# Kernel tuning notes

Hardware: AMD Instinct MI355X
Metric: run time of the kernel (lower is better)

## Reference

```python
import jax, jax.numpy as jnp
import numpy as np

B, V, C, CD, D, H, W = 1, 3, 32, 8, 32, 128, 160
LAMB = 1.5


def _bilinear(img, x, y):
    # img: [c, Hs, Ws]; x, y: pixel coords [D, HW]; zero padding, align_corners=True semantics
    c, Hs, Ws = img.shape
    x0 = jnp.floor(x)
    y0 = jnp.floor(y)
    x0i = x0.astype(jnp.int32)
    y0i = y0.astype(jnp.int32)
    wx = x - x0
    wy = y - y0
    imgf = img.reshape(c, Hs * Ws)

    def gather(xi, yi, w):
        valid = (xi >= 0) & (xi < Ws) & (yi >= 0) & (yi < Hs)
        lin = jnp.clip(yi, 0, Hs - 1) * Ws + jnp.clip(xi, 0, Ws - 1)
        v = jnp.take(imgf, lin.reshape(-1), axis=1).reshape((c,) + xi.shape)
        return v * (w * valid.astype(w.dtype))[None]

    return (gather(x0i, y0i, (1 - wx) * (1 - wy))
            + gather(x0i + 1, y0i, wx * (1 - wy))
            + gather(x0i, y0i + 1, (1 - wx) * wy)
            + gather(x0i + 1, y0i + 1, wx * wy))


def _homo_warp(src_fea, src_proj, ref_proj, depth_values):
    # src_fea [B,c,Hs,Ws]; projs [B,4,4]; depth_values [B,D,H,W] -> [B,c,D,H,W]
    b, c, Hs, Ws = src_fea.shape
    _, d, h, w = depth_values.shape
    proj = jnp.einsum('bij,bjk->bik', src_proj, jnp.linalg.inv(ref_proj))
    rot = proj[:, :3, :3]
    tr = proj[:, :3, 3]
    ys, xs = jnp.meshgrid(jnp.arange(h, dtype=src_fea.dtype), jnp.arange(w, dtype=src_fea.dtype), indexing='ij')
    xyz = jnp.stack([xs.reshape(-1), ys.reshape(-1), jnp.ones(h * w, dtype=src_fea.dtype)], 0)  # [3,HW]
    rx = jnp.einsum('bij,jn->bin', rot, xyz)  # [B,3,HW]
    dvals = depth_values.reshape(b, 1, d, h * w)
    pxyz = rx[:, :, None, :] * dvals + tr[:, :, None, None]  # [B,3,D,HW]
    z = pxyz[:, 2]
    px = pxyz[:, 0] / z  # [B,D,HW]
    py = pxyz[:, 1] / z
    out = jax.vmap(_bilinear)(src_fea, px, py)  # [B,c,D,HW]
    return out.reshape(b, c, d, h, w)


def setup_inputs() -> dict:
    key = jax.random.key(0)
    k1, k2, k3 = jax.random.split(key, 3)
    features = jax.random.normal(k1, (V, B, C, H, W), jnp.float32)
    deps_feature_stage = jax.random.normal(k2, (V, B, CD, H, W), jnp.float32)
    reg_w = jax.random.normal(k3, (1, C + CD), jnp.float32) * 0.1
    K = np.array([[200., 0., W / 2.], [0., 200., H / 2.], [0., 0., 1.]])
    mats = []
    for tx in [0.0, 1.0, -1.0]:
        Rt = np.eye(4)
        Rt[0, 3] = tx
        P = np.eye(4)
        P[:3, :4] = K @ Rt[:3, :4]
        mats.append(P)
    proj_matrices = jnp.asarray(np.stack(mats)[None], jnp.float32)  # [B,V,4,4]
    depth_values = jnp.broadcast_to(
        jnp.linspace(5.0, 10.0, D, dtype=jnp.float32)[None, :, None, None], (B, D, H, W)) + jnp.zeros((B, D, H, W), jnp.float32)
    return {'features': features, 'deps_feature_stage': deps_feature_stage,
            'proj_matrices': proj_matrices, 'depth_values': depth_values,
            'reg_w': reg_w, 'num_depth': D, 'stage_idx': 0}


def reference(features, deps_feature_stage, proj_matrices, depth_values, reg_w, num_depth, stage_idx):
    num_views = features.shape[0]
    d = depth_values.shape[1]
    ref_proj = proj_matrices[:, 0]

    def variance_volume(feats):
        ref = feats[0]  # [B,c,H,W]
        ref_vol = jnp.broadcast_to(ref[:, :, None], (ref.shape[0], ref.shape[1], d, ref.shape[2], ref.shape[3]))
        s = ref_vol
        sq = ref_vol * ref_vol
        for v in range(1, num_views):
            wv = _homo_warp(feats[v], proj_matrices[:, v], ref_proj, depth_values)
            s = s + wv
            sq = sq + wv * wv
        return sq / num_views - (s / num_views) ** 2

    volume_variance = variance_volume(features)      # [B,C,D,H,W]
    deps_variance = variance_volume(deps_feature_stage)  # [B,CD,D,H,W]
    var = jnp.concatenate([volume_variance, deps_variance], axis=1)
    # cost_regularization modeled as 1x1x1 conv reducing channels to 1
    cost = jnp.einsum('bcdhw,oc->bodhw', var, reg_w)[:, 0]  # [B,D,H,W]
    prob_volume = jax.nn.softmax(cost, axis=1)
    depth = jnp.sum(prob_volume * depth_values, axis=1)  # [B,H,W]
    samp_variance = (depth_values - depth[:, None]) ** 2
    exp_variance = LAMB * jnp.sqrt(jnp.sum(samp_variance * prob_volume, axis=1))
    return depth, exp_variance, prob_volume
```

## Files before the change

### kernel.cpp

```cpp
#include <hip/hip_runtime.h>
#include <hip/hip_fp16.h>
#include <math.h>

#define HH   128
#define WW   160
#define HWN  (HH*WW)
#define NCF  32
#define NCD  8
#define ND   32
#define NV   3
#define LAMBF 1.5f

template <int CH>
__device__ void transpose_tile(const float* __restrict__ src, __half* __restrict__ dst,
                               float (*lds)[33], int tid) {
    for (int i = tid; i < CH*8; i += 256) {
        int c = i >> 3, xg = (i & 7) << 2;
        *(float4*)&lds[c][xg] = *(const float4*)(src + c*HWN + xg);
    }
    __syncthreads();
    for (int i = tid; i < 32*(CH/4); i += 256) {
        int xl = i / (CH/4), c4 = (i % (CH/4)) * 4;
        __half2 h0 = __floats2half2_rn(lds[c4][xl],   lds[c4+1][xl]);
        __half2 h1 = __floats2half2_rn(lds[c4+2][xl], lds[c4+3][xl]);
        uint2 u; u.x = *(unsigned*)&h0; u.y = *(unsigned*)&h1;
        *(uint2*)(dst + xl*CH + c4) = u;
    }
}

__global__ __launch_bounds__(256) void prep_k(const float* __restrict__ feat,
                                              const float* __restrict__ deps,
                                              const float* __restrict__ proj,
                                              __half* __restrict__ featH,
                                              __half* __restrict__ depsH,
                                              float* __restrict__ projw) {
    if (blockIdx.x == 0 && blockIdx.y == 0 && blockIdx.z == 0 && threadIdx.x == 0) {
        float M00 = proj[0], M01 = proj[1], M02 = proj[2],  m0 = proj[3];
        float M10 = proj[4], M11 = proj[5], M12 = proj[6],  m1 = proj[7];
        float M20 = proj[8], M21 = proj[9], M22 = proj[10], m2 = proj[11];
        float c00 =  (M11*M22 - M12*M21);
        float c01 = -(M10*M22 - M12*M20);
        float c02 =  (M10*M21 - M11*M20);
        float det = M00*c00 + M01*c01 + M02*c02;
        float id  = 1.f / det;
        float i00 = c00*id, i01 = -(M01*M22 - M02*M21)*id, i02 =  (M01*M12 - M02*M11)*id;
        float i10 = c01*id, i11 =  (M00*M22 - M02*M20)*id, i12 = -(M00*M12 - M02*M10)*id;
        float i20 = c02*id, i21 = -(M00*M21 - M01*M20)*id, i22 =  (M00*M11 - M01*M10)*id;
        float t0 = -(i00*m0 + i01*m1 + i02*m2);
        float t1 = -(i10*m0 + i11*m1 + i12*m2);
        float t2 = -(i20*m0 + i21*m1 + i22*m2);
        #pragma unroll
        for (int v = 1; v < NV; v++) {
            const float* S = proj + v*16;
            float s00 = S[0], s01 = S[1], s02 = S[2],  st0 = S[3];
            float s10 = S[4], s11 = S[5], s12 = S[6],  st1 = S[7];
            float s20 = S[8], s21 = S[9], s22 = S[10], st2 = S[11];
            float* o = projw + (v-1)*12;
            o[0] = s00*i00 + s01*i10 + s02*i20;
            o[1] = s00*i01 + s01*i11 + s02*i21;
            o[2] = s00*i02 + s01*i12 + s02*i22;
            o[3] = s10*i00 + s11*i10 + s12*i20;
            o[4] = s10*i01 + s11*i11 + s12*i21;
            o[5] = s10*i02 + s11*i12 + s12*i22;
            o[6] = s20*i00 + s21*i10 + s22*i20;
            o[7] = s20*i01 + s21*i11 + s22*i21;
            o[8] = s20*i02 + s21*i12 + s22*i22;
            o[9]  = s00*t0 + s01*t1 + s02*t2 + st0;
            o[10] = s10*t0 + s11*t1 + s12*t2 + st1;
            o[11] = s20*t0 + s21*t1 + s22*t2 + st2;
        }
    }

    __shared__ float lds[NCF][33];
    const int z  = blockIdx.z;
    const int xb = blockIdx.x * 32;
    const int y  = blockIdx.y;
    if (z < NV) {
        transpose_tile<NCF>(feat + (size_t)(z*NCF)*HWN + y*WW + xb,
                            featH + (size_t)(z*HWN + y*WW + xb) * NCF,
                            lds, threadIdx.x);
    } else {
        transpose_tile<NCD>(deps + (size_t)((z - NV)*NCD)*HWN + y*WW + xb,
                            depsH + (size_t)((z - NV)*HWN + y*WW + xb) * NCD,
                            lds, threadIdx.x);
    }
}

__global__ __launch_bounds__(256) void cost_volume_k(
    const __half* __restrict__ featH,
    const __half* __restrict__ depsH,
    const float* __restrict__ dvals,
    const float* __restrict__ regw,
    const float* __restrict__ pws,
    float* __restrict__ out)
{
    __shared__ float cl [ND][9];
    __shared__ float dvl[ND][9];
    __shared__ float smax[8], sisum[8];

    const int t    = threadIdx.x;
    const int lane = t & 63;
    const int wid  = t >> 6;
    const int cg   = lane & 7;
    const int pl   = lane >> 3;
    const int pixg = blockIdx.x * 8 + pl;
    const int y    = pixg / WW;
    const int x    = pixg - y * WW;
    const float fx = (float)x, fy = (float)y;
    const int dbase = wid * 8;
    const int plbase = lane & 0x38;

    float RX[2], RY[2], RZ[2], T0[2], T1[2], T2[2];
    #pragma unroll
    for (int v = 0; v < 2; v++) {
        const float* q = pws + v*12;
        RX[v] = q[0]*fx + q[1]*fy + q[2];
        RY[v] = q[3]*fx + q[4]*fy + q[5];
        RZ[v] = q[6]*fx + q[7]*fy + q[8];
        T0[v] = q[9]; T1[v] = q[10]; T2[v] = q[11];
    }

    int SW00[2], SW10[2], SW01[2], SW11[2];
    int SO00[2], SO10[2], SO01[2], SO11[2];
    {
        float dvv_own = dvals[(dbase + cg)*HWN + pixg];
        dvl[dbase + cg][pl] = dvv_own;
        #pragma unroll
        for (int v = 0; v < 2; v++) {
            float pz = RZ[v]*dvv_own + T2[v];
            float iz = __builtin_amdgcn_rcpf(pz);
            float px = (RX[v]*dvv_own + T0[v]) * iz;
            float py = (RY[v]*dvv_own + T1[v]) * iz;
            float x0f = floorf(px), y0f = floorf(py);
            int x0 = (int)x0f, y0 = (int)y0f;
            float wx = px - x0f, wy = py - y0f;
            float omx = 1.f - wx, omy = 1.f - wy;
            bool vx0 = (x0 >= 0) & (x0 < WW);
            bool vx1 = (x0+1 >= 0) & (x0+1 < WW);
            bool vy0 = (y0 >= 0) & (y0 < HH);
            bool vy1 = (y0+1 >= 0) & (y0+1 < HH);
            float W00 = (vx0 && vy0) ? omx*omy : 0.f;
            float W10 = (vx1 && vy0) ? wx*omy  : 0.f;
            float W01 = (vx0 && vy1) ? omx*wy  : 0.f;
            float W11 = (vx1 && vy1) ? wx*wy   : 0.f;
            __half2 h;
            h = __float2half2_rn(W00); SW00[v] = *(int*)&h;
            h = __float2half2_rn(W10); SW10[v] = *(int*)&h;
            h = __float2half2_rn(W01); SW01[v] = *(int*)&h;
            h = __float2half2_rn(W11); SW11[v] = *(int*)&h;
            int xc0 = min(max(x0,   0), WW-1);
            int xc1 = min(max(x0+1, 0), WW-1);
            int yc0 = min(max(y0,   0), HH-1);
            int yc1 = min(max(y0+1, 0), HH-1);
            SO00[v] = (yc0*WW + xc0)*NCF;
            SO10[v] = (yc0*WW + xc1)*NCF;
            SO01[v] = (yc1*WW + xc0)*NCF;
            SO11[v] = (yc1*WW + xc1)*NCF;
        }
    }

    #define INTERP(BPTR, O00, O10, O01, O11, W00p, W10p, W01p, W11p)          \
        {                                                                      \
            uint2 u00 = *(const uint2*)(BPTR + O00);                           \
            uint2 u10 = *(const uint2*)(BPTR + O10);                           \
            uint2 u01 = *(const uint2*)(BPTR + O01);                           \
            uint2 u11 = *(const uint2*)(BPTR + O11);                           \
            __half2 wva = __hmul2(*(__half2*)&u00.x, W00p);                    \
            wva = __hfma2(*(__half2*)&u10.x, W10p, wva);                       \
            wva = __hfma2(*(__half2*)&u01.x, W01p, wva);                       \
            wva = __hfma2(*(__half2*)&u11.x, W11p, wva);                       \
            __half2 wvb = __hmul2(*(__half2*)&u00.y, W00p);                    \
            wvb = __hfma2(*(__half2*)&u10.y, W10p, wvb);                       \
            wvb = __hfma2(*(__half2*)&u01.y, W01p, wvb);                       \
            wvb = __hfma2(*(__half2*)&u11.y, W11p, wvb);                       \
            float2 fa = __half22float2(wva);                                   \
            float2 fb = __half22float2(wvb);                                   \
            s0 += fa.x; q0 = fmaf(fa.x, fa.x, q0);                             \
            s1 += fa.y; q1 = fmaf(fa.y, fa.y, q1);                             \
            s2 += fb.x; q2 = fmaf(fb.x, fb.x, q2);                             \
            s3 += fb.y; q3 = fmaf(fb.y, fb.y, q3);                             \
        }

    {
        uint2 ur = *(const uint2*)(featH + (size_t)pixg*NCF + cg*4);
        float2 ra = __half22float2(*(__half2*)&ur.x);
        float2 rb = __half22float2(*(__half2*)&ur.y);
        const float rx0 = ra.x, rx1 = ra.y, rx2 = rb.x, rx3 = rb.y;
        const float4 w4 = *(const float4*)(regw + cg*4);
        const float wca0 = w4.x*(1.f/3.f), wca1 = w4.y*(1.f/3.f),
                    wca2 = w4.z*(1.f/3.f), wca3 = w4.w*(1.f/3.f);
        const float wcb0 = w4.x*(1.f/9.f), wcb1 = w4.y*(1.f/9.f),
                    wcb2 = w4.z*(1.f/9.f), wcb3 = w4.w*(1.f/9.f);
        const __half* b1 = featH + (size_t)1*HWN*NCF + cg*4;
        const __half* b2 = featH + (size_t)2*HWN*NCF + cg*4;

        #pragma unroll 2
        for (int jj = 0; jj < 8; jj++) {
            const int src = plbase | jj;
            float s0 = rx0, s1 = rx1, s2 = rx2, s3 = rx3;
            float q0 = rx0*rx0, q1 = rx1*rx1, q2 = rx2*rx2, q3 = rx3*rx3;

            #pragma unroll
            for (int v = 0; v < 2; v++) {
                int w00i = __shfl(SW00[v], src, 64);
                int w10i = __shfl(SW10[v], src, 64);
                int w01i = __shfl(SW01[v], src, 64);
                int w11i = __shfl(SW11[v], src, 64);
                int o00  = __shfl(SO00[v], src, 64);
                int o10  = __shfl(SO10[v], src, 64);
                int o01  = __shfl(SO01[v], src, 64);
                int o11  = __shfl(SO11[v], src, 64);
                __half2 W00p = *(__half2*)&w00i, W10p = *(__half2*)&w10i;
                __half2 W01p = *(__half2*)&w01i, W11p = *(__half2*)&w11i;
                const __half* b = v ? b2 : b1;
                INTERP(b, o00, o10, o01, o11, W00p, W10p, W01p, W11p)
            }
            float part = wca0*q0 - wcb0*s0*s0;
            part = fmaf(wca1, q1, part); part = fmaf(-wcb1, s1*s1, part);
            part = fmaf(wca2, q2, part); part = fmaf(-wcb2, s2*s2, part);
            part = fmaf(wca3, q3, part); part = fmaf(-wcb3, s3*s3, part);
            part += __shfl_xor(part, 1);
            part += __shfl_xor(part, 2);
            part += __shfl_xor(part, 4);
            if (cg == jj) cl[dbase + jj][pl] = part;
        }
    }

    {
        const int cgd  = lane & 1;
        const int dsub = (lane >> 1) & 3;
        uint2 ur = *(const uint2*)(depsH + (size_t)pixg*NCD + cgd*4);
        float2 ra = __half22float2(*(__half2*)&ur.x);
        float2 rb = __half22float2(*(__half2*)&ur.y);
        const float rx0 = ra.x, rx1 = ra.y, rx2 = rb.x, rx3 = rb.y;
        const float4 w4 = *(const float4*)(regw + NCF + cgd*4);
        const float wca0 = w4.x*(1.f/3.f), wca1 = w4.y*(1.f/3.f),
                    wca2 = w4.z*(1.f/3.f), wca3 = w4.w*(1.f/3.f);
        const float wcb0 = w4.x*(1.f/9.f), wcb1 = w4.y*(1.f/9.f),
                    wcb2 = w4.z*(1.f/9.f), wcb3 = w4.w*(1.f/9.f);
        const __half* b1 = depsH + (size_t)1*HWN*NCD + cgd*4;
        const __half* b2 = depsH + (size_t)2*HWN*NCD + cgd*4;

        #pragma unroll
        for (int i = 0; i < 2; i++) {
            const int jj = dsub + 4*i;
            const int d  = dbase + jj;
            const int src = plbase | jj;
            float s0 = rx0, s1 = rx1, s2 = rx2, s3 = rx3;
            float q0 = rx0*rx0, q1 = rx1*rx1, q2 = rx2*rx2, q3 = rx3*rx3;

            #pragma unroll
            for (int v = 0; v < 2; v++) {
                int w00i = __shfl(SW00[v], src, 64);
                int w10i = __shfl(SW10[v], src, 64);
                int w01i = __shfl(SW01[v], src, 64);
                int w11i = __shfl(SW11[v], src, 64);
                int o00  = __shfl(SO00[v], src, 64) >> 2;
                int o10  = __shfl(SO10[v], src, 64) >> 2;
                int o01  = __shfl(SO01[v], src, 64) >> 2;
                int o11  = __shfl(SO11[v], src, 64) >> 2;
                __half2 W00p = *(__half2*)&w00i, W10p = *(__half2*)&w10i;
                __half2 W01p = *(__half2*)&w01i, W11p = *(__half2*)&w11i;
                const __half* b = v ? b2 : b1;
                INTERP(b, o00, o10, o01, o11, W00p, W10p, W01p, W11p)
            }
            float part = wca0*q0 - wcb0*s0*s0;
            part = fmaf(wca1, q1, part); part = fmaf(-wcb1, s1*s1, part);
            part = fmaf(wca2, q2, part); part = fmaf(-wcb2, s2*s2, part);
            part = fmaf(wca3, q3, part); part = fmaf(-wcb3, s3*s3, part);
            part += __shfl_xor(part, 1);
            if (cgd == 0) cl[d][pl] += part;
        }
    }
    __syncthreads();

    if (t < 8) {
        const int plx  = t;
        const int pixo = blockIdx.x * 8 + plx;
        float m = -1e30f;
        #pragma unroll
        for (int d = 0; d < ND; d++) m = fmaxf(m, cl[d][plx]);
        float sum = 0.f, pd = 0.f, pd2 = 0.f;
        #pragma unroll
        for (int d = 0; d < ND; d++) {
            float e   = __expf(cl[d][plx] - m);
            float dvv = dvl[d][plx];
            sum += e;
            pd  = fmaf(e, dvv, pd);
            pd2 = fmaf(e, dvv*dvv, pd2);
        }
        float isum  = 1.f / sum;
        float depth = pd * isum;
        float sv    = pd2 * isum - depth*depth;
        float ev    = LAMBF * sqrtf(fmaxf(sv, 0.f));
        smax[plx]  = m;
        sisum[plx] = isum;
        out[pixo]       = depth;
        out[HWN + pixo] = ev;
    }
    __syncthreads();
    {
        const int plx  = t & 7;
        const int dd   = t >> 3;
        const int pixo = blockIdx.x * 8 + plx;
        out[2*HWN + dd*HWN + pixo] = __expf(cl[dd][plx] - smax[plx]) * sisum[plx];
    }
}

extern "C" void kernel_launch(void* const* d_in, const int* in_sizes, int n_in,
                              void* d_out, int out_size, void* d_ws, size_t ws_size,
                              hipStream_t stream) {
    const float* features = (const float*)d_in[0];
    const float* deps     = (const float*)d_in[1];
    const float* proj     = (const float*)d_in[2];
    const float* dvals    = (const float*)d_in[3];
    const float* regw     = (const float*)d_in[4];

    float*  ws    = (float*)d_ws;
    float*  projw = ws;
    __half* featH = (__half*)(ws + 64);
    __half* depsH = featH + (size_t)NV*HWN*NCF;

    dim3 tg(WW/32, HH, 2*NV);
    prep_k<<<tg, 256, 0, stream>>>(features, deps, proj, featH, depsH, projw);

    cost_volume_k<<<HWN/8, 256, 0, stream>>>(featH, depsH, dvals, regw, projw,
                                             (float*)d_out);
}
```

Before: 103.0 us.

## Widen per-lane channel loads to 16 bytes and give the deps stage one depth per lane

The main feature stage now has each lane handle 8 half channels with uint4 loads and process two depths per group of 8 lanes, which halves the loop count and drops one shuffle-reduction step. The deps stage is restructured so each lane owns a whole depth and all 8 deps channels, using its own precomputed offsets and weights without any shuffles or cross-lane reduction. The goal is fewer, wider gather instructions and less shuffle overhead. The cost is more registers per thread, which may reduce occupancy.

```diff
diff --git a/kernel.cpp b/kernel.cpp
--- a/kernel.cpp
+++ b/kernel.cpp
@@ -101,7 +101,8 @@
     const int t    = threadIdx.x;
     const int lane = t & 63;
     const int wid  = t >> 6;
-    const int cg   = lane & 7;
+    const int cg2  = lane & 3;
+    const int dp   = (lane >> 2) & 1;
     const int pl   = lane >> 3;
     const int pixg = blockIdx.x * 8 + pl;
     const int y    = pixg / WW;
@@ -123,8 +124,8 @@
     int SW00[2], SW10[2], SW01[2], SW11[2];
     int SO00[2], SO10[2], SO01[2], SO11[2];
     {
-        float dvv_own = dvals[(dbase + cg)*HWN + pixg];
-        dvl[dbase + cg][pl] = dvv_own;
+        float dvv_own = dvals[(dbase + (lane & 7))*HWN + pixg];
+        dvl[dbase + (lane & 7)][pl] = dvv_own;
         #pragma unroll
         for (int v = 0; v < 2; v++) {
             float pz = RZ[v]*dvv_own + T2[v];
@@ -159,46 +160,48 @@
         }
     }
 
-    #define INTERP(BPTR, O00, O10, O01, O11, W00p, W10p, W01p, W11p)          \
-        {                                                                      \
-            uint2 u00 = *(const uint2*)(BPTR + O00);                           \
-            uint2 u10 = *(const uint2*)(BPTR + O10);                           \
-            uint2 u01 = *(const uint2*)(BPTR + O01);                           \
-            uint2 u11 = *(const uint2*)(BPTR + O11);                           \
-            __half2 wva = __hmul2(*(__half2*)&u00.x, W00p);                    \
-            wva = __hfma2(*(__half2*)&u10.x, W10p, wva);                       \
-            wva = __hfma2(*(__half2*)&u01.x, W01p, wva);                       \
-            wva = __hfma2(*(__half2*)&u11.x, W11p, wva);                       \
-            __half2 wvb = __hmul2(*(__half2*)&u00.y, W00p);                    \
-            wvb = __hfma2(*(__half2*)&u10.y, W10p, wvb);                       \
-            wvb = __hfma2(*(__half2*)&u01.y, W01p, wvb);                       \
-            wvb = __hfma2(*(__half2*)&u11.y, W11p, wvb);                       \
-            float2 fa = __half22float2(wva);                                   \
-            float2 fb = __half22float2(wvb);                                   \
-            s0 += fa.x; q0 = fmaf(fa.x, fa.x, q0);                             \
-            s1 += fa.y; q1 = fmaf(fa.y, fa.y, q1);                             \
-            s2 += fb.x; q2 = fmaf(fb.x, fb.x, q2);                             \
-            s3 += fb.y; q3 = fmaf(fb.y, fb.y, q3);                             \
-        }
+    #define H2OF(u, k) (((const __half2*)&(u))[k])
+    #define INTERP8(u00, u10, u01, u11, W00p, W10p, W01p, W11p)                \
+        { _Pragma("unroll")                                                    \
+          for (int k = 0; k < 4; k++) {                                        \
+            __half2 wv = __hmul2(H2OF(u00,k), W00p);                           \
+            wv = __hfma2(H2OF(u10,k), W10p, wv);                               \
+            wv = __hfma2(H2OF(u01,k), W01p, wv);                               \
+            wv = __hfma2(H2OF(u11,k), W11p, wv);                               \
+            float2 f = __half22float2(wv);                                     \
+            s[2*k]   += f.x; q[2*k]   = fmaf(f.x, f.x, q[2*k]);                \
+            s[2*k+1] += f.y; q[2*k+1] = fmaf(f.y, f.y, q[2*k+1]);              \
+          } }
 
     {
-        uint2 ur = *(const uint2*)(featH + (size_t)pixg*NCF + cg*4);
-        float2 ra = __half22float2(*(__half2*)&ur.x);
-        float2 rb = __half22float2(*(__half2*)&ur.y);
-        const float rx0 = ra.x, rx1 = ra.y, rx2 = rb.x, rx3 = rb.y;
-        const float4 w4 = *(const float4*)(regw + cg*4);
-        const float wca0 = w4.x*(1.f/3.f), wca1 = w4.y*(1.f/3.f),
-                    wca2 = w4.z*(1.f/3.f), wca3 = w4.w*(1.f/3.f);
-        const float wcb0 = w4.x*(1.f/9.f), wcb1 = w4.y*(1.f/9.f),
-                    wcb2 = w4.z*(1.f/9.f), wcb3 = w4.w*(1.f/9.f);
-        const __half* b1 = featH + (size_t)1*HWN*NCF + cg*4;
-        const __half* b2 = featH + (size_t)2*HWN*NCF + cg*4;
+        uint4 ur = *(const uint4*)(featH + (size_t)pixg*NCF + cg2*8);
+        float rx[8];
+        {
+            float2 f;
+            f = __half22float2(H2OF(ur,0)); rx[0]=f.x; rx[1]=f.y;
+            f = __half22float2(H2OF(ur,1)); rx[2]=f.x; rx[3]=f.y;
+            f = __half22float2(H2OF(ur,2)); rx[4]=f.x; rx[5]=f.y;
+            f = __half22float2(H2OF(ur,3)); rx[6]=f.x; rx[7]=f.y;
+        }
+        float wca[8], wcb[8];
+        {
+            float4 wa = *(const float4*)(regw + cg2*8);
+            float4 wb = *(const float4*)(regw + cg2*8 + 4);
+            wca[0]=wa.x*(1.f/3.f); wca[1]=wa.y*(1.f/3.f); wca[2]=wa.z*(1.f/3.f); wca[3]=wa.w*(1.f/3.f);
+            wca[4]=wb.x*(1.f/3.f); wca[5]=wb.y*(1.f/3.f); wca[6]=wb.z*(1.f/3.f); wca[7]=wb.w*(1.f/3.f);
+            wcb[0]=wa.x*(1.f/9.f); wcb[1]=wa.y*(1.f/9.f); wcb[2]=wa.z*(1.f/9.f); wcb[3]=wa.w*(1.f/9.f);
+            wcb[4]=wb.x*(1.f/9.f); wcb[5]=wb.y*(1.f/9.f); wcb[6]=wb.z*(1.f/9.f); wcb[7]=wb.w*(1.f/9.f);
+        }
+        const __half* b1 = featH + (size_t)1*HWN*NCF + cg2*8;
+        const __half* b2 = featH + (size_t)2*HWN*NCF + cg2*8;
 
         #pragma unroll 2
-        for (int jj = 0; jj < 8; jj++) {
+        for (int jp = 0; jp < 4; jp++) {
+            const int jj  = (dp << 2) | jp;
             const int src = plbase | jj;
-            float s0 = rx0, s1 = rx1, s2 = rx2, s3 = rx3;
-            float q0 = rx0*rx0, q1 = rx1*rx1, q2 = rx2*rx2, q3 = rx3*rx3;
+            float s[8], q[8];
+            #pragma unroll
+            for (int i = 0; i < 8; i++) { s[i] = rx[i]; q[i] = rx[i]*rx[i]; }
 
             #pragma unroll
             for (int v = 0; v < 2; v++) {
@@ -213,64 +216,70 @@
                 __half2 W00p = *(__half2*)&w00i, W10p = *(__half2*)&w10i;
                 __half2 W01p = *(__half2*)&w01i, W11p = *(__half2*)&w11i;
                 const __half* b = v ? b2 : b1;
-                INTERP(b, o00, o10, o01, o11, W00p, W10p, W01p, W11p)
+                uint4 u00 = *(const uint4*)(b + o00);
+                uint4 u10 = *(const uint4*)(b + o10);
+                uint4 u01 = *(const uint4*)(b + o01);
+                uint4 u11 = *(const uint4*)(b + o11);
+                INTERP8(u00, u10, u01, u11, W00p, W10p, W01p, W11p)
             }
-            float part = wca0*q0 - wcb0*s0*s0;
-            part = fmaf(wca1, q1, part); part = fmaf(-wcb1, s1*s1, part);
-            part = fmaf(wca2, q2, part); part = fmaf(-wcb2, s2*s2, part);
-            part = fmaf(wca3, q3, part); part = fmaf(-wcb3, s3*s3, part);
+            float part = wca[0]*q[0] - wcb[0]*s[0]*s[0];
+            #pragma unroll
+            for (int i = 1; i < 8; i++) {
+                part = fmaf(wca[i], q[i], part);
+                part = fmaf(-wcb[i], s[i]*s[i], part);
+            }
             part += __shfl_xor(part, 1);
             part += __shfl_xor(part, 2);
-            part += __shfl_xor(part, 4);
-            if (cg == jj) cl[dbase + jj][pl] = part;
+            if (cg2 == 0) cl[dbase + jj][pl] = part;
         }
     }
 
     {
-        const int cgd  = lane & 1;
-        const int dsub = (lane >> 1) & 3;
-        uint2 ur = *(const uint2*)(depsH + (size_t)pixg*NCD + cgd*4);
-        float2 ra = __half22float2(*(__half2*)&ur.x);
-        float2 rb = __half22float2(*(__half2*)&ur.y);
-        const float rx0 = ra.x, rx1 = ra.y, rx2 = rb.x, rx3 = rb.y;
-        const float4 w4 = *(const float4*)(regw + NCF + cgd*4);
-        const float wca0 = w4.x*(1.f/3.f), wca1 = w4.y*(1.f/3.f),
-                    wca2 = w4.z*(1.f/3.f), wca3 = w4.w*(1.f/3.f);
-        const float wcb0 = w4.x*(1.f/9.f), wcb1 = w4.y*(1.f/9.f),
-                    wcb2 = w4.z*(1.f/9.f), wcb3 = w4.w*(1.f/9.f);
-        const __half* b1 = depsH + (size_t)1*HWN*NCD + cgd*4;
-        const __half* b2 = depsH + (size_t)2*HWN*NCD + cgd*4;
-
-        #pragma unroll
-        for (int i = 0; i < 2; i++) {
-            const int jj = dsub + 4*i;
-            const int d  = dbase + jj;
-            const int src = plbase | jj;
-            float s0 = rx0, s1 = rx1, s2 = rx2, s3 = rx3;
-            float q0 = rx0*rx0, q1 = rx1*rx1, q2 = rx2*rx2, q3 = rx3*rx3;
-
-            #pragma unroll
-            for (int v = 0; v < 2; v++) {
-                int w00i = __shfl(SW00[v], src, 64);
-                int w10i = __shfl(SW10[v], src, 64);
-                int w01i = __shfl(SW01[v], src, 64);
-                int w11i = __shfl(SW11[v], src, 64);
-                int o00  = __shfl(SO00[v], src, 64) >> 2;
-                int o10  = __shfl(SO10[v], src, 64) >> 2;
-                int o01  = __shfl(SO01[v], src, 64) >> 2;
-                int o11  = __shfl(SO11[v], src, 64) >> 2;
-                __half2 W00p = *(__half2*)&w00i, W10p = *(__half2*)&w10i;
-                __half2 W01p = *(__half2*)&w01i, W11p = *(__half2*)&w11i;
-                const __half* b = v ? b2 : b1;
-                INTERP(b, o00, o10, o01, o11, W00p, W10p, W01p, W11p)
-            }
-            float part = wca0*q0 - wcb0*s0*s0;
-            part = fmaf(wca1, q1, part); part = fmaf(-wcb1, s1*s1, part);
-            part = fmaf(wca2, q2, part); part = fmaf(-wcb2, s2*s2, part);
-            part = fmaf(wca3, q3, part); part = fmaf(-wcb3, s3*s3, part);
-            part += __shfl_xor(part, 1);
-            if (cgd == 0) cl[d][pl] += part;
-        }
+        const int d = dbase + (lane & 7);
+        uint4 ur = *(const uint4*)(depsH + (size_t)pixg*NCD);
+        float rx[8];
+        {
+            float2 f;
+            f = __half22float2(H2OF(ur,0)); rx[0]=f.x; rx[1]=f.y;
+            f = __half22float2(H2OF(ur,1)); rx[2]=f.x; rx[3]=f.y;
+            f = __half22float2(H2OF(ur,2)); rx[4]=f.x; rx[5]=f.y;
+            f = __half22float2(H2OF(ur,3)); rx[6]=f.x; rx[7]=f.y;
+        }
+        float wca[8], wcb[8];
+        {
+            float4 wa = *(const float4*)(regw + NCF);
+            float4 wb = *(const float4*)(regw + NCF + 4);
+            wca[0]=wa.x*(1.f/3.f); wca[1]=wa.y*(1.f/3.f); wca[2]=wa.z*(1.f/3.f); wca[3]=wa.w*(1.f/3.f);
+            wca[4]=wb.x*(1.f/3.f); wca[5]=wb.y*(1.f/3.f); wca[6]=wb.z*(1.f/3.f); wca[7]=wb.w*(1.f/3.f);
+            wcb[0]=wa.x*(1.f/9.f); wcb[1]=wa.y*(1.f/9.f); wcb[2]=wa.z*(1.f/9.f); wcb[3]=wa.w*(1.f/9.f);
+            wcb[4]=wb.x*(1.f/9.f); wcb[5]=wb.y*(1.f/9.f); wcb[6]=wb.z*(1.f/9.f); wcb[7]=wb.w*(1.f/9.f);
+        }
+        float s[8], q[8];
+        #pragma unroll
+        for (int i = 0; i < 8; i++) { s[i] = rx[i]; q[i] = rx[i]*rx[i]; }
+
+        #pragma unroll
+        for (int v = 0; v < 2; v++) {
+            int o00 = SO00[v] >> 2;
+            int o10 = SO10[v] >> 2;
+            int o01 = SO01[v] >> 2;
+            int o11 = SO11[v] >> 2;
+            __half2 W00p = *(__half2*)&SW00[v], W10p = *(__half2*)&SW10[v];
+            __half2 W01p = *(__half2*)&SW01[v], W11p = *(__half2*)&SW11[v];
+            const __half* b = depsH + (size_t)(v+1)*HWN*NCD;
+            uint4 u00 = *(const uint4*)(b + o00);
+            uint4 u10 = *(const uint4*)(b + o10);
+            uint4 u01 = *(const uint4*)(b + o01);
+            uint4 u11 = *(const uint4*)(b + o11);
+            INTERP8(u00, u10, u01, u11, W00p, W10p, W01p, W11p)
+        }
+        float part = wca[0]*q[0] - wcb[0]*s[0]*s[0];
+        #pragma unroll
+        for (int i = 1; i < 8; i++) {
+            part = fmaf(wca[i], q[i], part);
+            part = fmaf(-wcb[i], s[i]*s[i], part);
+        }
+        cl[d][pl] += part;
     }
     __syncthreads();
 
```

New measurement: 94.31 us. -8.5%, faster.
